# Kernel optimization log

Measured on AMD Instinct MI355X. Metric: run time of the kernel, lower is better.

The kernel has to match this reference:

```python
import jax, jax.numpy as jnp
import numpy as np

# (C,H,W) of x0..x11; flattened size +1 homogeneous coordinate per key
SHAPES = [(3,32,32),(96,32,32),(96,32,32),(96,16,16),(192,16,16),(192,16,16),(192,8,8),(192,8,8),(192,8,8),(640,1,1),(100,1,1),(10,1,1)]
# (Cin,Cout,k,stride,pad) for conv1..conv9
CONV = [(3,96,3,1,1),(96,96,3,1,1),(96,96,3,2,1),(96,192,3,1,1),(192,192,3,1,1),(192,192,3,2,1),(192,192,3,1,1),(192,192,1,1,0),(192,10,1,1,0)]
B = 128


def setup_inputs():
    key = jax.random.key(0)
    inp = {}
    k, key = jax.random.split(key)
    inp['x0'] = jax.random.normal(k, (int(np.prod(SHAPES[0])) + 1, B), jnp.float32)
    for i, s in enumerate(SHAPES):
        n = int(np.prod(s)) + 1
        k1, k2, key = jax.random.split(key, 3)
        inp['perm%d' % i] = jax.random.permutation(k1, n)
        inp['diag%d' % i] = jax.random.uniform(k2, (n,), jnp.float32, 0.5, 1.5)
    for j, (ci, co, ks, st, pd) in enumerate(CONV):
        k1, k2, key = jax.random.split(key, 3)
        inp['w%d' % (j + 1)] = jax.random.normal(k1, (co, ci, ks, ks), jnp.float32) / np.float32(np.sqrt(ci * ks * ks))
        inp['b%d' % (j + 1)] = jax.random.normal(k2, (co,), jnp.float32) * 0.01
    k1, k2, k3, k4 = jax.random.split(key, 4)
    inp['fw1'] = jax.random.normal(k1, (100, 640), jnp.float32) / np.float32(np.sqrt(640))
    inp['fb1'] = jax.random.normal(k2, (100,), jnp.float32) * 0.01
    inp['fw2'] = jax.random.normal(k3, (10, 100), jnp.float32) / np.float32(np.sqrt(100))
    inp['fb2'] = jax.random.normal(k4, (10,), jnp.float32) * 0.01
    return inp


def _decode(x, perm, diag):
    # A_inv @ x with A_inv = P^T D^{-1}; P^T gather index is argsort(perm)
    return (x / diag[:, None])[jnp.argsort(perm)]


def _encode(y, perm, diag):
    # A @ y with A = D P; (P y)[i] = y[perm[i]]
    return diag[:, None] * y[perm]


def _conv_aug(v, w, b, shape_in, stride, pad):
    # affine-augmented conv: [W b; 0 1] applied to [feat; t]
    C, H, Wd = shape_in
    feat, t = v[:-1], v[-1]                      # (C*H*W, B), (B,)
    x = feat.T.reshape(-1, C, H, Wd)
    y = jax.lax.conv_general_dilated(x, w, (stride, stride), [(pad, pad), (pad, pad)],
                                     dimension_numbers=('NCHW', 'OIHW', 'NCHW'))
    y = y + b[None, :, None, None] * t[:, None, None, None]
    yf = y.reshape(y.shape[0], -1).T             # (N_out, B)
    return jnp.concatenate([yf, t[None, :]], axis=0)


def _fc_aug(v, w, b):
    feat, t = v[:-1], v[-1]
    return jnp.concatenate([w @ feat + b[:, None] * t[None, :], t[None, :]], axis=0)


def _forward(x0, perms, diags, ws, bs, fw1, fb1, fw2, fb2):
    x = x0
    for i in range(9):
        v = _decode(x, perms[i], diags[i])
        y = _conv_aug(v, ws[i], bs[i], SHAPES[i], CONV[i][3], CONV[i][4])
        x = jax.nn.relu(_encode(y, perms[i + 1], diags[i + 1]))
    v = _decode(x, perms[9], diags[9])
    x = jax.nn.relu(_encode(_fc_aug(v, fw1, fb1), perms[10], diags[10]))
    v = _decode(x, perms[10], diags[10])
    return _encode(_fc_aug(v, fw2, fb2), perms[11], diags[11])


def reference(x0, perm0, perm1, perm2, perm3, perm4, perm5, perm6, perm7, perm8, perm9, perm10, perm11,
              diag0, diag1, diag2, diag3, diag4, diag5, diag6, diag7, diag8, diag9, diag10, diag11,
              w1, b1, w2, b2, w3, b3, w4, b4, w5, b5, w6, b6, w7, b7, w8, b8, w9, b9,
              fw1, fb1, fw2, fb2):
    perms = [perm0, perm1, perm2, perm3, perm4, perm5, perm6, perm7, perm8, perm9, perm10, perm11]
    diags = [diag0, diag1, diag2, diag3, diag4, diag5, diag6, diag7, diag8, diag9, diag10, diag11]
    ws = [w1, w2, w3, w4, w5, w6, w7, w8, w9]
    bs = [b1, b2, b3, b4, b5, b6, b7, b8, b9]
    return _forward(x0, perms, diags, ws, bs, fw1, fb1, fw2, fb2)
```

## Files before the change

### kernel.cpp

```cpp
#include <hip/hip_runtime.h>


#define B 128
#define ZPAD 2048

typedef _Float16 f16_t;
typedef __attribute__((ext_vector_type(8))) _Float16 f16x8;
typedef __attribute__((ext_vector_type(4))) _Float16 f16x4;
typedef __attribute__((ext_vector_type(4))) float f32x4;


__global__ void decode_pack_kernel(const float* __restrict__ x, const int* __restrict__ perm,
                                   const float* __restrict__ diag,
                                   f16_t* __restrict__ xout, float* __restrict__ tout) {
    int row = blockIdx.x * 2 + (threadIdx.x >> 7);
    if (row >= 3073) return;
    int n = threadIdx.x & 127;
    int i = perm[row];
    float val = x[(size_t)row * B + n] / diag[row];
    if (i < 3072) {
        int c = i >> 10, p = i & 1023;
        xout[ZPAD + p * 1024 + n * 8 + c] = (f16_t)val;
    } else {
        tout[n] = val;
    }
}


__global__ void fc_kernel(const float* __restrict__ v, const float* __restrict__ w,
                          const float* __restrict__ b, float* __restrict__ y,
                          int K, int R, int do_relu) {
    int r = blockIdx.x;
    int n = threadIdx.x;
    float t = v[(size_t)K * B + n];
    float val;
    if (r == R) {
        val = t;
    } else {
        float a0 = 0.f, a1 = 0.f, a2 = 0.f, a3 = 0.f;
        float a4 = 0.f, a5 = 0.f, a6 = 0.f, a7 = 0.f;
        const float* wr = w + (size_t)r * K;
        int k = 0;
        for (; k + 8 <= K; k += 8) {
            float4 w0 = *(const float4*)(wr + k);
            float4 w1 = *(const float4*)(wr + k + 4);
            float x0 = v[(size_t)(k + 0) * B + n];
            float x1 = v[(size_t)(k + 1) * B + n];
            float x2 = v[(size_t)(k + 2) * B + n];
            float x3 = v[(size_t)(k + 3) * B + n];
            float x4 = v[(size_t)(k + 4) * B + n];
            float x5 = v[(size_t)(k + 5) * B + n];
            float x6 = v[(size_t)(k + 6) * B + n];
            float x7 = v[(size_t)(k + 7) * B + n];
            a0 = fmaf(w0.x, x0, a0);
            a1 = fmaf(w0.y, x1, a1);
            a2 = fmaf(w0.z, x2, a2);
            a3 = fmaf(w0.w, x3, a3);
            a4 = fmaf(w1.x, x4, a4);
            a5 = fmaf(w1.y, x5, a5);
            a6 = fmaf(w1.z, x6, a6);
            a7 = fmaf(w1.w, x7, a7);
        }
        for (; k < K; ++k)
            a0 = fmaf(wr[k], v[(size_t)k * B + n], a0);
        val = b[r] * t + ((a0 + a1) + (a2 + a3)) + ((a4 + a5) + (a6 + a7));
    }
    if (do_relu) val = fmaxf(val, 0.f);
    y[(size_t)r * B + n] = val;
}

__global__ void fc2_encode_kernel(const float* __restrict__ v, const float* __restrict__ w,
                                  const float* __restrict__ b, const int* __restrict__ perm,
                                  const float* __restrict__ diag, float* __restrict__ out) {
    int jrow = blockIdx.x;
    int n = threadIdx.x;
    int r = perm[jrow];
    float d = diag[jrow];
    float t = v[100 * B + n];
    float val;
    if (r == 10) {
        val = t;
    } else {
        float a0 = 0.f, a1 = 0.f, a2 = 0.f, a3 = 0.f;
        const float* wr = w + (size_t)r * 100;
        for (int k = 0; k < 100; k += 4) {
            float4 w4 = *(const float4*)(wr + k);
            a0 = fmaf(w4.x, v[(size_t)(k + 0) * B + n], a0);
            a1 = fmaf(w4.y, v[(size_t)(k + 1) * B + n], a1);
            a2 = fmaf(w4.z, v[(size_t)(k + 2) * B + n], a2);
            a3 = fmaf(w4.w, v[(size_t)(k + 3) * B + n], a3);
        }
        val = b[r] * t + (a0 + a1) + (a2 + a3);
    }
    out[(size_t)jrow * B + n] = d * val;
}


struct WArgs {
    const float* w[9]; const float* b[9];
    int Ci[9], Co[9], KS[9], Cp[9], NCG[9];
    int woff[10]; int boff[10];
};

__global__ void pack_weights_kernel(WArgs A, f16_t* __restrict__ wp, float* __restrict__ bp,
                                    f16_t* __restrict__ x8a, f16_t* __restrict__ x8b) {
    int idx = blockIdx.x * 256 + threadIdx.x;
    if (idx < ZPAD + 1048576) x8a[idx] = (f16_t)0.f;
    if (idx < ZPAD) x8b[idx] = (f16_t)0.f;
    if (idx < A.boff[9]) {
        int l = 0;
        while (idx >= A.boff[l + 1]) ++l;
        int co = idx - A.boff[l];
        bp[idx] = (co < A.Co[l]) ? A.b[l][co] : 0.f;
    }
    if (idx >= A.woff[9]) return;
    int l = 0;
    while (idx >= A.woff[l + 1]) ++l;
    int e = idx - A.woff[l];
    int j = e & 7;
    int t1 = e >> 3;
    int Cp = A.Cp[l];
    int co = t1 % Cp;
    int gg = t1 / Cp;
    int ncg = A.NCG[l];
    int tap = gg / ncg, cg = gg - tap * ncg;
    int ks = A.KS[l];
    int kh = tap / ks, kw = tap - kh * ks;
    int ci = cg * 8 + j;
    float val = 0.f;
    if (co < A.Co[l] && tap < ks * ks && ci < A.Ci[l])
        val = A.w[l][(((size_t)co * A.Ci[l] + ci) * ks + kh) * ks + kw];
    wp[idx] = (f16_t)val;
}


template <int KS, int NS, int NSPLIT, int CBW, bool F32OUT>
__global__ __launch_bounds__(64 * CBW) void conv_mfma_kernel(
    const f16_t* __restrict__ xin, const float* __restrict__ t_in,
    const f16_t* __restrict__ wp, const float* __restrict__ bp,
    f16_t* __restrict__ xout, float* __restrict__ t_out, float* __restrict__ f32out,
    int Hi, int Wi, int Wo_log2, int HWo,
    int stride, int pad, int NCG, int nchunk, int KGr, int Co, int Co_pad,
    int PB8, int CB)
{
    constexpr int PF = 2;
    constexpr int MS = 4;
    const int wave = threadIdx.x >> 6;
    const int lane = threadIdx.x & 63;
    const int q = lane >> 4;
    const int r = lane & 15;

    const int gb = blockIdx.x;
    const int xcd = gb & 7;
    int j = gb >> 3;
    int nh = 0, cog, p;
    if (NSPLIT > 1) { nh = j % NSPLIT; j /= NSPLIT; }
    if (CBW > 1) {
        cog = wave;
        p = xcd * PB8 + j;
    } else {
        cog = j % CB;
        p = xcd * PB8 + j / CB;
    }
    const int co0 = cog * 64;
    const int ncol0 = nh * (NS * 16);
    const int ncol8 = ncol0 * 8;

    const int ho = p >> Wo_log2;
    const int wo = p & ((1 << Wo_log2) - 1);
    const f16_t* xdata = xin + ZPAD;

    float tv[NS];
#pragma unroll
    for (int ns = 0; ns < NS; ++ns) tv[ns] = t_in[ncol0 + ns * 16 + r];

    f32x4 acc[MS][NS];
#pragma unroll
    for (int ms = 0; ms < MS; ++ms) {
        float4 b4 = *(const float4*)(bp + co0 + ms * 16 + q * 4);
#pragma unroll
        for (int ns = 0; ns < NS; ++ns) {
            acc[ms][ns][0] = b4.x * tv[ns];
            acc[ms][ns][1] = b4.y * tv[ns];
            acc[ms][ns][2] = b4.z * tv[ns];
            acc[ms][ns][3] = b4.w * tv[ns];
        }
    }

    const int hb = ho * stride - pad, wb = wo * stride - pad;
    const int HiWi = Hi * Wi;
    const int HiWi4 = 4 * HiWi;
    const int NCGHW = NCG * HiWi;
    const int wend = wb + KS;

    int g = q, cg = q, hi = hb, wi = wb, cgHW;
    {
        while (cg >= NCG) { cg -= NCG; ++wi; if (wi == wend) { wi = wb; ++hi; } }
        cgHW = cg * HiWi;
    }

    f16x8 bf[PF][NS], af[PF][MS];

    auto advance = [&]() {
        g += 4; cg += 4; cgHW += HiWi4;
        if (NCG >= 4) {
            int c2 = cg - NCG;
            bool wrap = c2 >= 0;
            int wn = wi + 1;
            bool ww = wrap & (wn == wend);
            cg   = wrap ? c2 : cg;
            cgHW = wrap ? cgHW - NCGHW : cgHW;
            wi   = wrap ? (ww ? wb : wn) : wi;
            hi   = ww ? hi + 1 : hi;
        } else {
            while (cg >= NCG) { cg -= NCG; cgHW -= NCGHW; ++wi; if (wi == wend) { wi = wb; ++hi; } }
        }
    };
    auto loadB = [&](f16x8* b) {
        bool v = (g < KGr) & ((unsigned)hi < (unsigned)Hi) & ((unsigned)wi < (unsigned)Wi);
        int boff = (cgHW + hi * Wi + wi) << 10;
        const f16_t* bb = xdata + (v ? boff : -ZPAD) + ncol8 + r * 8;
#pragma unroll
        for (int ns = 0; ns < NS; ++ns) b[ns] = *(const f16x8*)(bb + ns * 128);
    };
    auto loadA = [&](f16x8* a, int c) {
        int ac = c < nchunk ? c : nchunk - 1;
        const f16_t* ap = wp + (((ac * 4 + q) * Co_pad) + co0 + r) * 8;
#pragma unroll
        for (int ms = 0; ms < MS; ++ms) a[ms] = *(const f16x8*)(ap + ms * 128);
    };
    auto domfma = [&](f16x8* a, f16x8* b) {
#pragma unroll
        for (int ms = 0; ms < MS; ++ms)
#pragma unroll
            for (int ns = 0; ns < NS; ++ns)
                acc[ms][ns] = __builtin_amdgcn_mfma_f32_16x16x32_f16(a[ms], b[ns], acc[ms][ns], 0, 0, 0);
    };

#pragma unroll
    for (int pf = 0; pf < PF; ++pf) { loadB(bf[pf]); loadA(af[pf], pf); advance(); }
    const int nck = ((nchunk + PF - 1) / PF) * PF;
    for (int c = 0; c < nck; c += PF) {
#pragma unroll
        for (int pf = 0; pf < PF; ++pf) {
            domfma(af[pf], bf[pf]);
            loadB(bf[pf]); loadA(af[pf], c + PF + pf); advance();
        }
    }

    if (!F32OUT) {
#pragma unroll
        for (int ms = 0; ms < MS; ++ms) {
            int cob = co0 + ms * 16 + q * 4;
            if (cob < Co) {
                int off0 = ((cob >> 3) * HWo + p) * 1024 + (cob & 7) + ncol8 + r * 8;
#pragma unroll
                for (int ns = 0; ns < NS; ++ns) {
                    f16x4 h;
                    h[0] = (f16_t)fmaxf(acc[ms][ns][0], 0.f);
                    h[1] = (f16_t)fmaxf(acc[ms][ns][1], 0.f);
                    h[2] = (f16_t)fmaxf(acc[ms][ns][2], 0.f);
                    h[3] = (f16_t)fmaxf(acc[ms][ns][3], 0.f);
                    *(f16x4*)(xout + ZPAD + off0 + ns * 128) = h;
                }
            }
        }
        if (gb == 0) {
            for (int i = threadIdx.x; i < B; i += 64 * CBW)
                t_out[i] = fmaxf(t_in[i], 0.f);
        }
    } else {
#pragma unroll
        for (int ms = 0; ms < MS; ++ms)
#pragma unroll
            for (int ns = 0; ns < NS; ++ns)
#pragma unroll
                for (int e = 0; e < 4; ++e) {
                    int co = co0 + ms * 16 + q * 4 + e;
                    if (co < Co)
                        f32out[((size_t)co * HWo + p) * B + ncol0 + ns * 16 + r] =
                            fmaxf(acc[ms][ns][e], 0.f);
                }
        if (gb == 0) {
            for (int i = threadIdx.x; i < B; i += 64 * CBW)
                f32out[(size_t)Co * HWo * B + i] = fmaxf(t_in[i], 0.f);
        }
    }
}


extern "C" void kernel_launch(void* const* d_in, const int* in_sizes, int n_in,
                              void* d_out, int out_size, void* d_ws, size_t ws_size,
                              hipStream_t stream) {
    const float* x0 = (const float*)d_in[0];
    const int*   perm[12];
    const float* diag[12];
    for (int i = 0; i < 12; ++i) {
        perm[i] = (const int*)d_in[1 + 2 * i];
        diag[i] = (const float*)d_in[2 + 2 * i];
    }
    const float* wts[9];
    const float* bia[9];
    for (int j = 0; j < 9; ++j) {
        wts[j] = (const float*)d_in[25 + 2 * j];
        bia[j] = (const float*)d_in[26 + 2 * j];
    }
    const float* fw1 = (const float*)d_in[43];
    const float* fb1 = (const float*)d_in[44];
    const float* fw2 = (const float*)d_in[45];
    const float* fb2 = (const float*)d_in[46];
    float* out = (float*)d_out;

    static const int CiA[9]  = {3, 96, 96, 96, 192, 192, 192, 192, 192};
    static const int CoA[9]  = {96, 96, 96, 192, 192, 192, 192, 192, 10};
    static const int KSA[9]  = {3, 3, 3, 3, 3, 3, 3, 1, 1};
    static const int CpA[9]  = {128, 128, 128, 192, 192, 192, 192, 192, 64};
    static const int NCGA[9] = {1, 12, 12, 12, 24, 24, 24, 24, 24};
    static const int KGRA[9] = {9, 108, 108, 108, 216, 216, 216, 24, 24};
    static const int NCHK[9] = {3, 27, 27, 27, 54, 54, 54, 6, 6};
    static const int HiA[9]  = {32, 32, 32, 16, 16, 16, 8, 8, 8};
    static const int WoL[9]  = {5, 5, 4, 4, 4, 3, 3, 3, 3};
    static const int HWoA[9] = {1024, 1024, 256, 256, 256, 64, 64, 64, 64};
    static const int STA[9]  = {1, 1, 2, 1, 1, 2, 1, 1, 1};
    static const int PDA[9]  = {1, 1, 1, 1, 1, 1, 1, 0, 0};

    char* wsb = (char*)d_ws;
    const size_t BUF_F32  = 1574912;
    const size_t X8_BYTES = (size_t)(ZPAD + 12 * 1024 * 1024) * 2;
    float* bufA = (float*)wsb;
    float* bufB = (float*)(wsb + BUF_F32);
    f16_t* x8a  = (f16_t*)(wsb + 2 * BUF_F32);
    f16_t* x8b  = (f16_t*)(wsb + 2 * BUF_F32 + X8_BYTES);
    f16_t* wpb  = (f16_t*)(wsb + 2 * BUF_F32 + 2 * X8_BYTES);
    const size_t WP_BYTES = 2888704;
    float* bpb  = (float*)(wsb + 2 * BUF_F32 + 2 * X8_BYTES + WP_BYTES);
    float* t0   = (float*)((char*)bpb + 8192);
    float* t1   = t0 + 256;

    WArgs WA;
    int wo = 0, bo = 0;
    for (int l = 0; l < 9; ++l) {
        WA.w[l] = wts[l]; WA.b[l] = bia[l];
        WA.Ci[l] = CiA[l]; WA.Co[l] = CoA[l]; WA.KS[l] = KSA[l];
        WA.Cp[l] = CpA[l]; WA.NCG[l] = NCGA[l];
        WA.woff[l] = wo; wo += NCHK[l] * 4 * CpA[l] * 8;
        WA.boff[l] = bo; bo += CpA[l];
    }
    WA.woff[9] = wo; WA.boff[9] = bo;
    pack_weights_kernel<<<(wo + 255) / 256, 256, 0, stream>>>(WA, wpb, bpb, x8a, x8b);

    decode_pack_kernel<<<(3073 + 1) / 2, 256, 0, stream>>>(x0, perm[0], diag[0], x8a, t0);

    f16_t* xin = x8a; f16_t* xout = x8b;
    float* tin = t0;  float* tout = t1;
    for (int l = 0; l < 9; ++l) {
        const int PB8 = HWoA[l] / 8;
        const int CB = CpA[l] / 64;
        const f16_t* wpl = wpb + WA.woff[l];
        const float* bpl = bpb + WA.boff[l];
        if (l <= 1) {
            conv_mfma_kernel<3, 8, 1, 2, false><<<8 * PB8, 128, 0, stream>>>(
                xin, tin, wpl, bpl, xout, tout, nullptr,
                HiA[l], HiA[l], WoL[l], HWoA[l], STA[l], PDA[l],
                NCGA[l], NCHK[l], KGRA[l], CoA[l], CpA[l], PB8, CB);
        } else if (l == 2) {
            conv_mfma_kernel<3, 4, 2, 2, false><<<8 * PB8 * 2, 128, 0, stream>>>(
                xin, tin, wpl, bpl, xout, tout, nullptr,
                HiA[l], HiA[l], WoL[l], HWoA[l], STA[l], PDA[l],
                NCGA[l], NCHK[l], KGRA[l], CoA[l], CpA[l], PB8, CB);
        } else if (l <= 4) {
            conv_mfma_kernel<3, 8, 1, 3, false><<<8 * PB8, 192, 0, stream>>>(
                xin, tin, wpl, bpl, xout, tout, nullptr,
                HiA[l], HiA[l], WoL[l], HWoA[l], STA[l], PDA[l],
                NCGA[l], NCHK[l], KGRA[l], CoA[l], CpA[l], PB8, CB);
        } else if (l <= 6) {
            conv_mfma_kernel<3, 2, 4, 1, false><<<8 * PB8 * CB * 4, 64, 0, stream>>>(
                xin, tin, wpl, bpl, xout, tout, nullptr,
                HiA[l], HiA[l], WoL[l], HWoA[l], STA[l], PDA[l],
                NCGA[l], NCHK[l], KGRA[l], CoA[l], CpA[l], PB8, CB);
        } else if (l == 7) {
            conv_mfma_kernel<1, 2, 4, 1, false><<<8 * PB8 * CB * 4, 64, 0, stream>>>(
                xin, tin, wpl, bpl, xout, tout, nullptr,
                HiA[l], HiA[l], WoL[l], HWoA[l], STA[l], PDA[l],
                NCGA[l], NCHK[l], KGRA[l], CoA[l], CpA[l], PB8, CB);
        } else {
            conv_mfma_kernel<1, 2, 4, 1, true><<<8 * PB8 * CB * 4, 64, 0, stream>>>(
                xin, tin, wpl, bpl, nullptr, nullptr, bufA,
                HiA[l], HiA[l], WoL[l], HWoA[l], STA[l], PDA[l],
                NCGA[l], NCHK[l], KGRA[l], CoA[l], CpA[l], PB8, CB);
        }
        f16_t* xt = xin; xin = xout; xout = xt;
        float* tt = tin; tin = tout; tout = tt;
    }

    fc_kernel<<<101, B, 0, stream>>>(bufA, fw1, fb1, bufB, 640, 100, 1);
    fc2_encode_kernel<<<11, B, 0, stream>>>(bufB, fw2, fb2, perm[11], diag[11], out);
}
```

Measured before the change: 321.7 us.

## Fuse tail conv layers and FC head into one cooperative kernel

```diff
diff --git a/kernel.cpp b/kernel.cpp
--- a/kernel.cpp
+++ b/kernel.cpp
@@ -1,4 +1,7 @@
 #include <hip/hip_runtime.h>
+#include <hip/hip_cooperative_groups.h>
+
+namespace cg = cooperative_groups;
 
 
 #define B 128
@@ -24,75 +27,6 @@
     } else {
         tout[n] = val;
     }
-}
-
-
-__global__ void fc_kernel(const float* __restrict__ v, const float* __restrict__ w,
-                          const float* __restrict__ b, float* __restrict__ y,
-                          int K, int R, int do_relu) {
-    int r = blockIdx.x;
-    int n = threadIdx.x;
-    float t = v[(size_t)K * B + n];
-    float val;
-    if (r == R) {
-        val = t;
-    } else {
-        float a0 = 0.f, a1 = 0.f, a2 = 0.f, a3 = 0.f;
-        float a4 = 0.f, a5 = 0.f, a6 = 0.f, a7 = 0.f;
-        const float* wr = w + (size_t)r * K;
-        int k = 0;
-        for (; k + 8 <= K; k += 8) {
-            float4 w0 = *(const float4*)(wr + k);
-            float4 w1 = *(const float4*)(wr + k + 4);
-            float x0 = v[(size_t)(k + 0) * B + n];
-            float x1 = v[(size_t)(k + 1) * B + n];
-            float x2 = v[(size_t)(k + 2) * B + n];
-            float x3 = v[(size_t)(k + 3) * B + n];
-            float x4 = v[(size_t)(k + 4) * B + n];
-            float x5 = v[(size_t)(k + 5) * B + n];
-            float x6 = v[(size_t)(k + 6) * B + n];
-            float x7 = v[(size_t)(k + 7) * B + n];
-            a0 = fmaf(w0.x, x0, a0);
-            a1 = fmaf(w0.y, x1, a1);
-            a2 = fmaf(w0.z, x2, a2);
-            a3 = fmaf(w0.w, x3, a3);
-            a4 = fmaf(w1.x, x4, a4);
-            a5 = fmaf(w1.y, x5, a5);
-            a6 = fmaf(w1.z, x6, a6);
-            a7 = fmaf(w1.w, x7, a7);
-        }
-        for (; k < K; ++k)
-            a0 = fmaf(wr[k], v[(size_t)k * B + n], a0);
-        val = b[r] * t + ((a0 + a1) + (a2 + a3)) + ((a4 + a5) + (a6 + a7));
-    }
-    if (do_relu) val = fmaxf(val, 0.f);
-    y[(size_t)r * B + n] = val;
-}
-
-__global__ void fc2_encode_kernel(const float* __restrict__ v, const float* __restrict__ w,
-                                  const float* __restrict__ b, const int* __restrict__ perm,
-                                  const float* __restrict__ diag, float* __restrict__ out) {
-    int jrow = blockIdx.x;
-    int n = threadIdx.x;
-    int r = perm[jrow];
-    float d = diag[jrow];
-    float t = v[100 * B + n];
-    float val;
-    if (r == 10) {
-        val = t;
-    } else {
-        float a0 = 0.f, a1 = 0.f, a2 = 0.f, a3 = 0.f;
-        const float* wr = w + (size_t)r * 100;
-        for (int k = 0; k < 100; k += 4) {
-            float4 w4 = *(const float4*)(wr + k);
-            a0 = fmaf(w4.x, v[(size_t)(k + 0) * B + n], a0);
-            a1 = fmaf(w4.y, v[(size_t)(k + 1) * B + n], a1);
-            a2 = fmaf(w4.z, v[(size_t)(k + 2) * B + n], a2);
-            a3 = fmaf(w4.w, v[(size_t)(k + 3) * B + n], a3);
-        }
-        val = b[r] * t + (a0 + a1) + (a2 + a3);
-    }
-    out[(size_t)jrow * B + n] = d * val;
 }
 
 
@@ -289,6 +223,232 @@
 }
 
 
+template <int KS, int NS, int NSPLIT, int CB, bool F32OUT,
+          int HI, int WOL, int HWO, int STRIDE, int PAD,
+          int NCGk, int NCHUNK, int KGR, int CO, int CP>
+__device__ __forceinline__ void conv_task(
+    int gb, int lane,
+    const f16_t* __restrict__ xin, const float* __restrict__ t_in,
+    const f16_t* __restrict__ wp, const float* __restrict__ bp,
+    f16_t* __restrict__ xout, float* __restrict__ t_out, float* __restrict__ f32out)
+{
+    constexpr int PF = 2;
+    constexpr int MS = 4;
+    constexpr int PB8 = HWO / 8;
+    const int q = lane >> 4;
+    const int r = lane & 15;
+
+    const int xcd = gb & 7;
+    int j = gb >> 3;
+    int nh = 0;
+    if (NSPLIT > 1) { nh = j % NSPLIT; j /= NSPLIT; }
+    const int cog = j % CB;
+    const int p = xcd * PB8 + j / CB;
+    const int co0 = cog * 64;
+    const int ncol0 = nh * (NS * 16);
+    const int ncol8 = ncol0 * 8;
+
+    const int ho = p >> WOL;
+    const int wo = p & ((1 << WOL) - 1);
+    const f16_t* xdata = xin + ZPAD;
+
+    float tv[NS];
+#pragma unroll
+    for (int ns = 0; ns < NS; ++ns) tv[ns] = t_in[ncol0 + ns * 16 + r];
+
+    f32x4 acc[MS][NS];
+#pragma unroll
+    for (int ms = 0; ms < MS; ++ms) {
+        float4 b4 = *(const float4*)(bp + co0 + ms * 16 + q * 4);
+#pragma unroll
+        for (int ns = 0; ns < NS; ++ns) {
+            acc[ms][ns][0] = b4.x * tv[ns];
+            acc[ms][ns][1] = b4.y * tv[ns];
+            acc[ms][ns][2] = b4.z * tv[ns];
+            acc[ms][ns][3] = b4.w * tv[ns];
+        }
+    }
+
+    const int hb = ho * STRIDE - PAD, wb = wo * STRIDE - PAD;
+    constexpr int HiWi = HI * HI;
+    constexpr int HiWi4 = 4 * HiWi;
+    constexpr int NCGHW = NCGk * HiWi;
+    const int wend = wb + KS;
+
+    int g = q, cg = q, hi = hb, wi = wb, cgHW = q * HiWi;
+
+    f16x8 bf[PF][NS], af[PF][MS];
+
+    auto advance = [&]() {
+        g += 4; cg += 4; cgHW += HiWi4;
+        int c2 = cg - NCGk;
+        bool wrap = c2 >= 0;
+        int wn = wi + 1;
+        bool ww = wrap & (wn == wend);
+        cg   = wrap ? c2 : cg;
+        cgHW = wrap ? cgHW - NCGHW : cgHW;
+        wi   = wrap ? (ww ? wb : wn) : wi;
+        hi   = ww ? hi + 1 : hi;
+    };
+    auto loadB = [&](f16x8* b) {
+        bool v = (g < KGR) & ((unsigned)hi < (unsigned)HI) & ((unsigned)wi < (unsigned)HI);
+        int boff = (cgHW + hi * HI + wi) << 10;
+        const f16_t* bb = xdata + (v ? boff : -ZPAD) + ncol8 + r * 8;
+#pragma unroll
+        for (int ns = 0; ns < NS; ++ns) b[ns] = *(const f16x8*)(bb + ns * 128);
+    };
+    auto loadA = [&](f16x8* a, int c) {
+        int ac = c < NCHUNK ? c : NCHUNK - 1;
+        const f16_t* ap = wp + (((ac * 4 + q) * CP) + co0 + r) * 8;
+#pragma unroll
+        for (int ms = 0; ms < MS; ++ms) a[ms] = *(const f16x8*)(ap + ms * 128);
+    };
+    auto domfma = [&](f16x8* a, f16x8* b) {
+#pragma unroll
+        for (int ms = 0; ms < MS; ++ms)
+#pragma unroll
+            for (int ns = 0; ns < NS; ++ns)
+                acc[ms][ns] = __builtin_amdgcn_mfma_f32_16x16x32_f16(a[ms], b[ns], acc[ms][ns], 0, 0, 0);
+    };
+
+#pragma unroll
+    for (int pf = 0; pf < PF; ++pf) { loadB(bf[pf]); loadA(af[pf], pf); advance(); }
+    constexpr int NCK = ((NCHUNK + PF - 1) / PF) * PF;
+    for (int c = 0; c < NCK; c += PF) {
+#pragma unroll
+        for (int pf = 0; pf < PF; ++pf) {
+            domfma(af[pf], bf[pf]);
+            loadB(bf[pf]); loadA(af[pf], c + PF + pf); advance();
+        }
+    }
+
+    if (!F32OUT) {
+#pragma unroll
+        for (int ms = 0; ms < MS; ++ms) {
+            int cob = co0 + ms * 16 + q * 4;
+            if (cob < CO) {
+                int off0 = ((cob >> 3) * HWO + p) * 1024 + (cob & 7) + ncol8 + r * 8;
+#pragma unroll
+                for (int ns = 0; ns < NS; ++ns) {
+                    f16x4 h;
+                    h[0] = (f16_t)fmaxf(acc[ms][ns][0], 0.f);
+                    h[1] = (f16_t)fmaxf(acc[ms][ns][1], 0.f);
+                    h[2] = (f16_t)fmaxf(acc[ms][ns][2], 0.f);
+                    h[3] = (f16_t)fmaxf(acc[ms][ns][3], 0.f);
+                    *(f16x4*)(xout + ZPAD + off0 + ns * 128) = h;
+                }
+            }
+        }
+        if (gb == 0) {
+            for (int i = lane; i < B; i += 64)
+                t_out[i] = fmaxf(t_in[i], 0.f);
+        }
+    } else {
+#pragma unroll
+        for (int ms = 0; ms < MS; ++ms)
+#pragma unroll
+            for (int ns = 0; ns < NS; ++ns)
+#pragma unroll
+                for (int e = 0; e < 4; ++e) {
+                    int co = co0 + ms * 16 + q * 4 + e;
+                    if (co < CO)
+                        f32out[((size_t)co * HWO + p) * B + ncol0 + ns * 16 + r] =
+                            fmaxf(acc[ms][ns][e], 0.f);
+                }
+        if (gb == 0) {
+            for (int i = lane; i < B; i += 64)
+                f32out[(size_t)CO * HWO * B + i] = fmaxf(t_in[i], 0.f);
+        }
+    }
+}
+
+
+__global__ __launch_bounds__(64) void tail_fused_kernel(
+    const f16_t* __restrict__ wp, const float* __restrict__ bp,
+    f16_t* __restrict__ xa, f16_t* __restrict__ xb,
+    float* __restrict__ bufA, float* __restrict__ bufB,
+    float* __restrict__ t0, float* __restrict__ t1,
+    const float* __restrict__ fw1, const float* __restrict__ fb1,
+    const float* __restrict__ fw2, const float* __restrict__ fb2,
+    const int* __restrict__ perm11, const float* __restrict__ diag11,
+    float* __restrict__ out)
+{
+    cg::grid_group grid = cg::this_grid();
+    const int gb = blockIdx.x;
+    const int lane = threadIdx.x;
+
+    conv_task<3, 2, 4, 3, false, 16, 3, 64, 2, 1, 24, 54, 216, 192, 192>(
+        gb, lane, xb, t1, wp + 731136, bp + 768, xa, t0, nullptr);
+    __threadfence(); grid.sync();
+
+    conv_task<3, 2, 4, 3, false, 8, 3, 64, 1, 1, 24, 54, 216, 192, 192>(
+        gb, lane, xa, t0, wp + 1062912, bp + 960, xb, t1, nullptr);
+    __threadfence(); grid.sync();
+
+    conv_task<1, 2, 4, 3, false, 8, 3, 64, 1, 0, 24, 6, 24, 192, 192>(
+        gb, lane, xb, t1, wp + 1394688, bp + 1152, xa, t0, nullptr);
+    __threadfence(); grid.sync();
+
+    if (gb < 256)
+        conv_task<1, 2, 4, 1, true, 8, 3, 64, 1, 0, 24, 6, 24, 10, 64>(
+            gb, lane, xa, t0, wp + 1431552, bp + 1344, nullptr, nullptr, bufA);
+    __threadfence(); grid.sync();
+
+    if (gb < 202) {
+        int rr = gb >> 1;
+        int n = ((gb & 1) << 6) | lane;
+        float t = bufA[640 * B + n];
+        float val;
+        if (rr == 100) {
+            val = t;
+        } else {
+            float a0 = 0.f, a1 = 0.f, a2 = 0.f, a3 = 0.f;
+            float a4 = 0.f, a5 = 0.f, a6 = 0.f, a7 = 0.f;
+            const float* wr = fw1 + (size_t)rr * 640;
+            for (int k = 0; k < 640; k += 8) {
+                float4 w0 = *(const float4*)(wr + k);
+                float4 w1 = *(const float4*)(wr + k + 4);
+                a0 = fmaf(w0.x, bufA[(size_t)(k + 0) * B + n], a0);
+                a1 = fmaf(w0.y, bufA[(size_t)(k + 1) * B + n], a1);
+                a2 = fmaf(w0.z, bufA[(size_t)(k + 2) * B + n], a2);
+                a3 = fmaf(w0.w, bufA[(size_t)(k + 3) * B + n], a3);
+                a4 = fmaf(w1.x, bufA[(size_t)(k + 4) * B + n], a4);
+                a5 = fmaf(w1.y, bufA[(size_t)(k + 5) * B + n], a5);
+                a6 = fmaf(w1.z, bufA[(size_t)(k + 6) * B + n], a6);
+                a7 = fmaf(w1.w, bufA[(size_t)(k + 7) * B + n], a7);
+            }
+            val = fb1[rr] * t + ((a0 + a1) + (a2 + a3)) + ((a4 + a5) + (a6 + a7));
+        }
+        bufB[(size_t)rr * B + n] = fmaxf(val, 0.f);
+    }
+    __threadfence(); grid.sync();
+
+    if (gb < 22) {
+        int jrow = gb >> 1;
+        int n = ((gb & 1) << 6) | lane;
+        int rr = perm11[jrow];
+        float d = diag11[jrow];
+        float t = bufB[100 * B + n];
+        float val;
+        if (rr == 10) {
+            val = t;
+        } else {
+            float a0 = 0.f, a1 = 0.f, a2 = 0.f, a3 = 0.f;
+            const float* wr = fw2 + (size_t)rr * 100;
+            for (int k = 0; k < 100; k += 4) {
+                float4 w4 = *(const float4*)(wr + k);
+                a0 = fmaf(w4.x, bufB[(size_t)(k + 0) * B + n], a0);
+                a1 = fmaf(w4.y, bufB[(size_t)(k + 1) * B + n], a1);
+                a2 = fmaf(w4.z, bufB[(size_t)(k + 2) * B + n], a2);
+                a3 = fmaf(w4.w, bufB[(size_t)(k + 3) * B + n], a3);
+            }
+            val = fb2[rr] * t + (a0 + a1) + (a2 + a3);
+        }
+        out[(size_t)jrow * B + n] = d * val;
+    }
+}
+
+
 extern "C" void kernel_launch(void* const* d_in, const int* in_sizes, int n_in,
                               void* d_out, int out_size, void* d_ws, size_t ws_size,
                               hipStream_t stream) {
@@ -353,7 +513,7 @@
 
     f16_t* xin = x8a; f16_t* xout = x8b;
     float* tin = t0;  float* tout = t1;
-    for (int l = 0; l < 9; ++l) {
+    for (int l = 0; l < 5; ++l) {
         const int PB8 = HWoA[l] / 8;
         const int CB = CpA[l] / 64;
         const f16_t* wpl = wpb + WA.woff[l];
@@ -368,31 +528,28 @@
                 xin, tin, wpl, bpl, xout, tout, nullptr,
                 HiA[l], HiA[l], WoL[l], HWoA[l], STA[l], PDA[l],
                 NCGA[l], NCHK[l], KGRA[l], CoA[l], CpA[l], PB8, CB);
-        } else if (l <= 4) {
-            conv_mfma_kernel<3, 8, 1, 3, false><<<8 * PB8, 192, 0, stream>>>(
+        } else {
+            conv_mfma_kernel<3, 4, 2, 3, false><<<8 * PB8 * 2, 192, 0, stream>>>(
                 xin, tin, wpl, bpl, xout, tout, nullptr,
                 HiA[l], HiA[l], WoL[l], HWoA[l], STA[l], PDA[l],
                 NCGA[l], NCHK[l], KGRA[l], CoA[l], CpA[l], PB8, CB);
-        } else if (l <= 6) {
-            conv_mfma_kernel<3, 2, 4, 1, false><<<8 * PB8 * CB * 4, 64, 0, stream>>>(
-                xin, tin, wpl, bpl, xout, tout, nullptr,
-                HiA[l], HiA[l], WoL[l], HWoA[l], STA[l], PDA[l],
-                NCGA[l], NCHK[l], KGRA[l], CoA[l], CpA[l], PB8, CB);
-        } else if (l == 7) {
-            conv_mfma_kernel<1, 2, 4, 1, false><<<8 * PB8 * CB * 4, 64, 0, stream>>>(
-                xin, tin, wpl, bpl, xout, tout, nullptr,
-                HiA[l], HiA[l], WoL[l], HWoA[l], STA[l], PDA[l],
-                NCGA[l], NCHK[l], KGRA[l], CoA[l], CpA[l], PB8, CB);
-        } else {
-            conv_mfma_kernel<1, 2, 4, 1, true><<<8 * PB8 * CB * 4, 64, 0, stream>>>(
-                xin, tin, wpl, bpl, nullptr, nullptr, bufA,
-                HiA[l], HiA[l], WoL[l], HWoA[l], STA[l], PDA[l],
-                NCGA[l], NCHK[l], KGRA[l], CoA[l], CpA[l], PB8, CB);
         }
         f16_t* xt = xin; xin = xout; xout = xt;
         float* tt = tin; tin = tout; tout = tt;
     }
 
-    fc_kernel<<<101, B, 0, stream>>>(bufA, fw1, fb1, bufB, 640, 100, 1);
-    fc2_encode_kernel<<<11, B, 0, stream>>>(bufB, fw2, fb2, perm[11], diag[11], out);
+    {
+        void* ka0 = (void*)wpb;  void* ka1 = (void*)bpb;
+        void* ka2 = (void*)x8a;  void* ka3 = (void*)x8b;
+        void* ka4 = (void*)bufA; void* ka5 = (void*)bufB;
+        void* ka6 = (void*)t0;   void* ka7 = (void*)t1;
+        void* ka8 = (void*)fw1;  void* ka9 = (void*)fb1;
+        void* ka10 = (void*)fw2; void* ka11 = (void*)fb2;
+        void* ka12 = (void*)perm[11]; void* ka13 = (void*)diag[11];
+        void* ka14 = (void*)out;
+        void* args[15] = { &ka0, &ka1, &ka2, &ka3, &ka4, &ka5, &ka6, &ka7,
+                           &ka8, &ka9, &ka10, &ka11, &ka12, &ka13, &ka14 };
+        hipLaunchCooperativeKernel((const void*)tail_fused_kernel,
+                                   dim3(768), dim3(64), args, 0, stream);
+    }
 }
```

After: 917.1 us. 2.85x slower.
